# Performance work log

Measured on AMD Instinct MI355X. Metric: run time of the kernel, lower is better.

Reference implementation:

```python
import jax, jax.numpy as jnp
import numpy as np

EPS = 1e-5
EMBED_DIM = 1024
CTX_DIM = 768
NUM_HEADS = 16
DH = EMBED_DIM // NUM_HEADS
# Faithful to torch source: embed_dim // num_heads ** 0.5 parses as embed_dim // (num_heads**0.5)
SCALE = EMBED_DIM // (NUM_HEADS ** 0.5)  # = 256.0


def ws_conv1x1(x, w, b, mask):
    # weight-standardized 1x1 conv1d: w [O, I, 1], x [B, I, T]
    w2 = w[..., 0]
    mu = jnp.mean(w2, axis=1, keepdims=True)
    var = jnp.var(w2, axis=1, keepdims=True)
    wn = (w2 - mu) * jax.lax.rsqrt(var + EPS)
    y = jnp.einsum('oi,bit->bot', wn, x) + b[None, :, None]
    if mask is not None:
        y = jnp.where(mask, y, 0.0)  # mask [B,1,T] bool
    return y


def layernorm(x, g, b):
    # normalize over last axis
    mu = jnp.mean(x, axis=-1, keepdims=True)
    var = jnp.var(x, axis=-1, keepdims=True)
    return (x - mu) * jax.lax.rsqrt(var + EPS) * g + b


def setup_inputs() -> dict:
    key = jax.random.key(0)
    ks = jax.random.split(key, 16)
    B, T, S = 4, 1024, 1024
    inp = {
        'x': jax.random.normal(ks[0], (B, EMBED_DIM, T), dtype=jnp.float32),
        'context': jax.random.normal(ks[1], (B, CTX_DIM, S), dtype=jnp.float32),
        'mask': jax.random.randint(ks[2], (B, 1, T), 0, 2).astype(bool),
        'mask_ctx': jax.random.randint(ks[3], (B, 1, S), 0, 2).astype(bool),
        'qw': jax.random.normal(ks[4], (EMBED_DIM, EMBED_DIM, 1), dtype=jnp.float32) * 0.02,
        'qb': jnp.zeros((EMBED_DIM,), jnp.float32),
        'kw': jax.random.normal(ks[5], (EMBED_DIM, CTX_DIM, 1), dtype=jnp.float32) * 0.02,
        'kb': jnp.zeros((EMBED_DIM,), jnp.float32),
        'vw': jax.random.normal(ks[6], (EMBED_DIM, CTX_DIM, 1), dtype=jnp.float32) * 0.02,
        'vb': jnp.zeros((EMBED_DIM,), jnp.float32),
        'ow': jax.random.normal(ks[7], (EMBED_DIM, EMBED_DIM, 1), dtype=jnp.float32) * 0.02,
        'ob': jnp.zeros((EMBED_DIM,), jnp.float32),
        'gq': jnp.ones((DH,), jnp.float32), 'bq': jnp.zeros((DH,), jnp.float32),
        'gk': jnp.ones((DH,), jnp.float32), 'bk': jnp.zeros((DH,), jnp.float32),
        'gv': jnp.ones((DH,), jnp.float32), 'bv': jnp.zeros((DH,), jnp.float32),
    }
    return inp


def reference(x, context, mask, mask_ctx, qw, qb, kw, kb, vw, vb, ow, ob, gq, bq, gk, bk, gv, bv):
    B, E, T = x.shape
    S = context.shape[-1]
    q = ws_conv1x1(x, qw, qb, mask)            # [B,E,T]
    k = ws_conv1x1(context, kw, kb, mask_ctx)  # [B,E,S]
    v = ws_conv1x1(context, vw, vb, mask_ctx)  # [B,E,S]
    # split heads -> [B,H,dh,L]
    q = q.reshape(B, NUM_HEADS, DH, T)
    k = k.reshape(B, NUM_HEADS, DH, S)
    v = v.reshape(B, NUM_HEADS, DH, S)
    # middle_norm: LayerNorm over dh (applied on transposed layout)
    q = jnp.swapaxes(layernorm(jnp.swapaxes(q, -1, -2), gq, bq), -1, -2)
    k = jnp.swapaxes(layernorm(jnp.swapaxes(k, -1, -2), gk, bk), -1, -2)
    v = jnp.swapaxes(layernorm(jnp.swapaxes(v, -1, -2), gv, bv), -1, -2)
    # scores: k^T @ q -> [B,H,S,T]
    scores = jnp.einsum('bhds,bhdt->bhst', k, q) / SCALE
    scores = jnp.where(mask[:, :, None, :], scores, -1e9)  # mask over query dim T
    scores = jax.nn.softmax(scores, axis=-1)               # softmax over T (as in source)
    scores = jnp.where(mask_ctx[:, :, :, None], scores, 0.0)
    out = jnp.einsum('bhds,bhst->bhdt', v, scores)          # v @ scores -> [B,H,dh,T]
    out = out.reshape(B, E, T)
    out = ws_conv1x1(out, ow, ob, mask) + x
    return out
```

## Files before the change

kernel.cpp:

```cpp
#include <hip/hip_runtime.h>

#define NB 4
#define TT 1024
#define SS 1024
#define EE 1024
#define CCH 768
#define NH 16
#define DHH 64
#define EPSF 1e-5f
#define QSCALE (1.4426950408889634f / 256.0f)

typedef unsigned short u16;
typedef __attribute__((ext_vector_type(8))) short short8;
typedef __attribute__((ext_vector_type(8))) unsigned short u16x8;
typedef __attribute__((ext_vector_type(4))) unsigned short u16x4;
typedef __attribute__((ext_vector_type(4))) float f32x4;

__device__ __forceinline__ u16 f2bu(float f) {
    union { float f; unsigned u; } x; x.f = f;
    unsigned r = x.u + 0x7fffu + ((x.u >> 16) & 1u);
    return (u16)(r >> 16);
}
__device__ __forceinline__ float bu2f(u16 u) {
    union { unsigned u; float f; } x; x.u = ((unsigned)u) << 16; return x.f;
}

#if __has_builtin(__builtin_amdgcn_exp2f)
#define EXP2(x) __builtin_amdgcn_exp2f(x)
#else
#define EXP2(x) exp2f(x)
#endif

#define MFMA16(a, b, c) __builtin_amdgcn_mfma_f32_16x16x32_bf16((a), (b), (c), 0, 0, 0)

__global__ __launch_bounds__(256) void ws_norm4(
    const float* __restrict__ qw, const float* __restrict__ kw,
    const float* __restrict__ vw, const float* __restrict__ ow,
    u16* __restrict__ wqn, u16* __restrict__ wkn,
    u16* __restrict__ wvn, u16* __restrict__ won) {
    int mat = blockIdx.y;
    const float* w = mat == 0 ? qw : (mat == 1 ? kw : (mat == 2 ? vw : ow));
    u16* wn = mat == 0 ? wqn : (mat == 1 ? wkn : (mat == 2 ? wvn : won));
    int I = (mat == 1 || mat == 2) ? CCH : EE;
    int row = blockIdx.x;
    const float* wr = w + (size_t)row * I;
    float s = 0.f, s2 = 0.f;
    for (int i = threadIdx.x; i < I; i += 256) { float v = wr[i]; s += v; s2 += v * v; }
#pragma unroll
    for (int off = 32; off > 0; off >>= 1) { s += __shfl_down(s, off); s2 += __shfl_down(s2, off); }
    __shared__ float sa[4], sb[4], smean, srstd;
    int wid = threadIdx.x >> 6;
    if ((threadIdx.x & 63) == 0) { sa[wid] = s; sb[wid] = s2; }
    __syncthreads();
    if (threadIdx.x == 0) {
        float ts = sa[0] + sa[1] + sa[2] + sa[3];
        float ts2 = sb[0] + sb[1] + sb[2] + sb[3];
        float mean = ts / (float)I;
        float var = ts2 / (float)I - mean * mean;
        smean = mean; srstd = rsqrtf(var + EPSF);
    }
    __syncthreads();
    float mean = smean, r = srstd;
    u16* wo = wn + (size_t)row * I;
    for (int i = threadIdx.x; i < I; i += 256) wo[i] = f2bu((wr[i] - mean) * r);
}

__global__ __launch_bounds__(256) void transpose2_f2b(
    const float* __restrict__ x, const float* __restrict__ ctx,
    u16* __restrict__ xT, u16* __restrict__ cT) {
    __shared__ float tile[64][65];
    int yy = blockIdx.y;
    int mat = yy < 16 ? 0 : 1;
    int r0 = (mat == 0 ? yy : yy - 16) * 64;
    int R = mat == 0 ? EE : CCH;
    const float* in = mat == 0 ? x : ctx;
    u16* out = mat == 0 ? xT : cT;
    int c0 = blockIdx.x * 64, b = blockIdx.z;
    const float* ip = in + (size_t)b * R * 1024;
    u16* op = out + (size_t)b * R * 1024;
    int tid = threadIdx.x;
#pragma unroll
    for (int m = 0; m < 16; m++) {
        int id = tid + 256 * m; int r = id >> 6, c = id & 63;
        tile[r][c] = ip[(size_t)(r0 + r) * 1024 + c0 + c];
    }
    __syncthreads();
#pragma unroll
    for (int m = 0; m < 16; m++) {
        int id = tid + 256 * m; int rr = id >> 6, cc = id & 63;
        op[(size_t)(c0 + rr) * R + r0 + cc] = f2bu(tile[cc][rr]);
    }
}

__device__ __forceinline__ void gemm_core(
    const u16* __restrict__ A, const u16* __restrict__ Bp, int I,
    int o0, int l0, u16 (*at)[72], u16 (*bt)[72], f32x4 (&acc)[4][2]) {
    int tid = threadIdx.x;
    int w = tid >> 6, lane = tid & 63, quad = lane >> 4, l16 = lane & 15;
    int wm = w & 1, wn = w >> 1;
    int rA = tid >> 3, cA = (tid & 7) * 8;
    u16x8 ra[2][4], rb[2][2];
#pragma unroll
    for (int p = 0; p < 2; p++) {
        int kb = p * 64;
#pragma unroll
        for (int m = 0; m < 4; m++)
            ra[p][m] = *(const u16x8*)&A[(size_t)(o0 + rA + 32 * m) * I + kb + cA];
#pragma unroll
        for (int m = 0; m < 2; m++)
            rb[p][m] = *(const u16x8*)&Bp[(size_t)(l0 + rA + 32 * m) * I + kb + cA];
    }
    for (int k0 = 0; k0 < I; k0 += 128) {
#pragma unroll
        for (int half = 0; half < 2; half++) {
            __syncthreads();
#pragma unroll
            for (int m = 0; m < 4; m++) *(u16x8*)&at[rA + 32 * m][cA] = ra[half][m];
#pragma unroll
            for (int m = 0; m < 2; m++) *(u16x8*)&bt[rA + 32 * m][cA] = rb[half][m];
            __syncthreads();
            int kpre = k0 + half * 64 + 128;
            if (kpre < I) {
#pragma unroll
                for (int m = 0; m < 4; m++)
                    ra[half][m] = *(const u16x8*)&A[(size_t)(o0 + rA + 32 * m) * I + kpre + cA];
#pragma unroll
                for (int m = 0; m < 2; m++)
                    rb[half][m] = *(const u16x8*)&Bp[(size_t)(l0 + rA + 32 * m) * I + kpre + cA];
            }
#pragma unroll
            for (int ks = 0; ks < 64; ks += 32) {
                short8 af[4], bf[2];
#pragma unroll
                for (int i = 0; i < 4; i++)
                    af[i] = *(const short8*)&at[wm * 64 + i * 16 + l16][ks + quad * 8];
#pragma unroll
                for (int j = 0; j < 2; j++)
                    bf[j] = *(const short8*)&bt[wn * 32 + j * 16 + l16][ks + quad * 8];
#pragma unroll
                for (int mt = 0; mt < 4; mt++)
#pragma unroll
                    for (int nt = 0; nt < 2; nt++)
                        acc[mt][nt] = MFMA16(af[mt], bf[nt], acc[mt][nt]);
            }
        }
    }
}

__global__ __launch_bounds__(256) void proj_qkv(
    const u16* __restrict__ wq, const u16* __restrict__ wk, const u16* __restrict__ wv,
    const u16* __restrict__ xT, const u16* __restrict__ cT,
    const float* __restrict__ qb, const float* __restrict__ kb, const float* __restrict__ vbi,
    const int* __restrict__ mask_t, const int* __restrict__ mask_c,
    const float* __restrict__ gq, const float* __restrict__ bq,
    const float* __restrict__ gk, const float* __restrict__ bk,
    u16* __restrict__ qT, u16* __restrict__ kT, u16* __restrict__ yv) {
    __shared__ u16 at[128][72];
    __shared__ u16 bt[64][72];
    __shared__ float sg[64], sbe[64], sbias[128];
    int tid = threadIdx.x;
    int w = tid >> 6, lane = tid & 63, quad = lane >> 4, l16 = lane & 15;
    int wm = w & 1, wn = w >> 1;
    int mat = blockIdx.y >> 3;
    int o0 = (blockIdx.y & 7) * 128;
    int l0 = blockIdx.x * 64;
    int b = blockIdx.z;
    const u16* A = mat == 0 ? wq : (mat == 1 ? wk : wv);
    const u16* BT = mat == 0 ? xT : cT;
    const float* bias = mat == 0 ? qb : (mat == 1 ? kb : vbi);
    const int* maskp = mat == 0 ? mask_t : mask_c;
    int I = mat == 0 ? EE : CCH;
    if (mat < 2 && tid < 64) {
        sg[tid] = (mat == 0 ? gq : gk)[tid];
        sbe[tid] = (mat == 0 ? bq : bk)[tid];
    }
    if (tid < 128) sbias[tid] = bias[o0 + tid];

    f32x4 acc[4][2] = {};
    gemm_core(A, BT + (size_t)b * 1024 * I, I, o0, l0, at, bt, acc);

    const int* mrow = maskp + (size_t)b * 1024;
    if (mat < 2) {
        u16* outT = mat == 0 ? qT : kT;
        float scale = mat == 0 ? QSCALE : 1.0f;
        int h = (o0 >> 6) + wm;
        int bh = b * NH + h;
#pragma unroll
        for (int nt = 0; nt < 2; nt++) {
            int l = l0 + wn * 32 + nt * 16 + l16;
            int mval = mrow[l];
            float vbuf[16];
            float s = 0.f;
#pragma unroll
            for (int mt = 0; mt < 4; mt++)
#pragma unroll
                for (int reg = 0; reg < 4; reg++) {
                    float v = mval ? (acc[mt][nt][reg] + sbias[wm * 64 + mt * 16 + quad * 4 + reg]) : 0.f;
                    vbuf[mt * 4 + reg] = v; s += v;
                }
            s += __shfl_xor(s, 16); s += __shfl_xor(s, 32);
            float mean = s * (1.f / 64);
            float s2 = 0.f;
#pragma unroll
            for (int i = 0; i < 16; i++) { float dv = vbuf[i] - mean; s2 += dv * dv; }
            s2 += __shfl_xor(s2, 16); s2 += __shfl_xor(s2, 32);
            float r = rsqrtf(s2 * (1.f / 64) + EPSF);
            u16* op = outT + ((size_t)bh * 1024 + l) * 64;
#pragma unroll
            for (int mt = 0; mt < 4; mt++) {
                u16x4 pk;
#pragma unroll
                for (int reg = 0; reg < 4; reg++) {
                    int d = mt * 16 + quad * 4 + reg;
                    pk[reg] = f2bu(((vbuf[mt * 4 + reg] - mean) * r * sg[d] + sbe[d]) * scale);
                }
                *(u16x4*)&op[mt * 16 + quad * 4] = pk;
            }
        }
    } else {
#pragma unroll
        for (int nt = 0; nt < 2; nt++) {
            int l = l0 + wn * 32 + nt * 16 + l16;
            int mval = mrow[l];
#pragma unroll
            for (int mt = 0; mt < 4; mt++)
#pragma unroll
                for (int reg = 0; reg < 4; reg++) {
                    int o = o0 + wm * 64 + mt * 16 + quad * 4 + reg;
                    float v = mval ? (acc[mt][nt][reg] + sbias[wm * 64 + mt * 16 + quad * 4 + reg]) : 0.f;
                    yv[((size_t)b * EE + o) * 1024 + l] = f2bu(v);
                }
        }
    }
}

__global__ __launch_bounds__(256) void proj_o(
    const u16* __restrict__ won, const u16* __restrict__ aT,
    const float* __restrict__ obi, const int* __restrict__ mask,
    const float* __restrict__ x, float* __restrict__ out) {
    __shared__ u16 at[128][72];
    __shared__ u16 bt[64][72];
    __shared__ float sbias[128];
    int tid = threadIdx.x;
    int w = tid >> 6, lane = tid & 63, quad = lane >> 4, l16 = lane & 15;
    int wm = w & 1, wn = w >> 1;
    int o0 = blockIdx.y * 128, l0 = blockIdx.x * 64, b = blockIdx.z;
    if (tid < 128) sbias[tid] = obi[o0 + tid];
    f32x4 acc[4][2] = {};
    gemm_core(won, aT + (size_t)b * TT * EE, EE, o0, l0, at, bt, acc);
    const int* mrow = mask + (size_t)b * TT;
#pragma unroll
    for (int nt = 0; nt < 2; nt++) {
        int l = l0 + wn * 32 + nt * 16 + l16;
        int mval = mrow[l];
#pragma unroll
        for (int mt = 0; mt < 4; mt++)
#pragma unroll
            for (int reg = 0; reg < 4; reg++) {
                int o = o0 + wm * 64 + mt * 16 + quad * 4 + reg;
                float v = mval ? (acc[mt][nt][reg] + sbias[wm * 64 + mt * 16 + quad * 4 + reg]) : 0.f;
                size_t off = ((size_t)b * EE + o) * TT + l;
                out[off] = v + x[off];
            }
    }
}

__global__ __launch_bounds__(256) void attn_stats_mfma(
    const u16* __restrict__ qT, const u16* __restrict__ kT,
    const int* __restrict__ mask, const int* __restrict__ mask_ctx,
    const float* __restrict__ gv, const float* __restrict__ bv,
    u16* __restrict__ yv) {
    __shared__ u16 kt[64][72];
    __shared__ u16 qt[64][72];
    __shared__ float lp[4][64];
    int tid = threadIdx.x;
    int w = tid >> 6, lane = tid & 63, quad = lane >> 4, l16 = lane & 15;
    int s0 = blockIdx.x * 64, h = blockIdx.y, b = blockIdx.z;
    int head = b * NH + h;
    const u16* kp = kT + (size_t)head * SS * DHH;
    const u16* qp = qT + (size_t)head * TT * DHH;
    const int* mk = mask + (size_t)b * TT;
    int rA = tid >> 3, cA = (tid & 7) * 8;
#pragma unroll
    for (int m = 0; m < 2; m++)
        *(u16x8*)&kt[rA + 32 * m][cA] = *(const u16x8*)&kp[(size_t)(s0 + rA + 32 * m) * DHH + cA];
    u16x8 rq[2][2];
#pragma unroll
    for (int p = 0; p < 2; p++)
#pragma unroll
        for (int m = 0; m < 2; m++)
            rq[p][m] = *(const u16x8*)&qp[(size_t)(p * 64 + rA + 32 * m) * DHH + cA];
    float rl[4][4] = {};
    for (int t0 = 0; t0 < TT; t0 += 128) {
#pragma unroll
        for (int half = 0; half < 2; half++) {
            int tb = t0 + half * 64;
            __syncthreads();
#pragma unroll
            for (int m = 0; m < 2; m++) *(u16x8*)&qt[rA + 32 * m][cA] = rq[half][m];
            __syncthreads();
            int tpre = tb + 128;
            if (tpre < TT) {
#pragma unroll
                for (int m = 0; m < 2; m++)
                    rq[half][m] = *(const u16x8*)&qp[(size_t)(tpre + rA + 32 * m) * DHH + cA];
            }
            int mval = mk[tb + w * 16 + l16];
            f32x4 acc[4] = {};
#pragma unroll
            for (int ks = 0; ks < 64; ks += 32) {
                short8 bf = *(const short8*)&qt[w * 16 + l16][ks + quad * 8];
#pragma unroll
                for (int mt = 0; mt < 4; mt++) {
                    short8 af = *(const short8*)&kt[mt * 16 + l16][ks + quad * 8];
                    acc[mt] = MFMA16(af, bf, acc[mt]);
                }
            }
            if (mval) {
#pragma unroll
                for (int mt = 0; mt < 4; mt++)
#pragma unroll
                    for (int reg = 0; reg < 4; reg++)
                        rl[mt][reg] += EXP2(acc[mt][reg]);
            }
        }
    }
#pragma unroll
    for (int mt = 0; mt < 4; mt++) {
#pragma unroll
        for (int reg = 0; reg < 4; reg++) {
            float v = rl[mt][reg];
            v += __shfl_xor(v, 1); v += __shfl_xor(v, 2);
            v += __shfl_xor(v, 4); v += __shfl_xor(v, 8);
            if (l16 == 0) lp[w][mt * 16 + quad * 4 + reg] = v;
        }
    }
    __syncthreads();
    if (tid < 64) {
        int s = s0 + tid;
        float lv = lp[0][tid] + lp[1][tid] + lp[2][tid] + lp[3][tid];
        int mc = mask_ctx[(size_t)b * SS + s];
        float wsc = (mc != 0 && lv > 0.f) ? (1.f / lv) : 0.f;
        u16* vcol = yv + ((size_t)b * EE + h * 64) * SS + s;
        float sm = 0.f, s2 = 0.f;
#pragma unroll
        for (int d = 0; d < DHH; d++) {
            float v = bu2f(vcol[(size_t)d * SS]);
            sm += v; s2 += v * v;
        }
        float mean = sm * (1.f / DHH);
        float var = s2 * (1.f / DHH) - mean * mean;
        float r = rsqrtf(var + EPSF);
#pragma unroll
        for (int d = 0; d < DHH; d++) {
            float v = bu2f(vcol[(size_t)d * SS]);
            vcol[(size_t)d * SS] = f2bu(((v - mean) * r * gv[d] + bv[d]) * wsc);
        }
    }
}

__global__ __launch_bounds__(256) void attn_pv_mfma(
    const u16* __restrict__ qT, const u16* __restrict__ kT, const u16* __restrict__ vs,
    const int* __restrict__ mask, u16* __restrict__ aT) {
    __shared__ u16 qt[64][72];
    __shared__ u16 kt[64][72];
    __shared__ u16 vt[64][72];
    __shared__ u16 pt[64][72];
    int tid = threadIdx.x;
    int w = tid >> 6, lane = tid & 63, quad = lane >> 4, l16 = lane & 15;
    int t0 = blockIdx.x * 64, h = blockIdx.y, b = blockIdx.z;
    int head = b * NH + h;
    const u16* qp = qT + (size_t)head * TT * DHH;
    const u16* kp = kT + (size_t)head * SS * DHH;
    const u16* vp = vs + ((size_t)head * DHH) * SS;
    int rA = tid >> 3, cA = (tid & 7) * 8;
#pragma unroll
    for (int m = 0; m < 2; m++)
        *(u16x8*)&qt[rA + 32 * m][cA] = *(const u16x8*)&qp[(size_t)(t0 + rA + 32 * m) * DHH + cA];
    u16x8 rk[2][2], rv[2][2];
#pragma unroll
    for (int p = 0; p < 2; p++)
#pragma unroll
        for (int m = 0; m < 2; m++) {
            rk[p][m] = *(const u16x8*)&kp[(size_t)(p * 64 + rA + 32 * m) * DHH + cA];
            rv[p][m] = *(const u16x8*)&vp[(size_t)(rA + 32 * m) * SS + p * 64 + cA];
        }
    int mkv = mask[(size_t)b * TT + t0 + w * 16 + l16];
    int tl = w * 16 + l16;

    f32x4 oacc[4] = {};
    for (int s0 = 0; s0 < SS; s0 += 128) {
#pragma unroll
        for (int half = 0; half < 2; half++) {
            int sb = s0 + half * 64;
            __syncthreads();
#pragma unroll
            for (int m = 0; m < 2; m++) {
                *(u16x8*)&kt[rA + 32 * m][cA] = rk[half][m];
                *(u16x8*)&vt[rA + 32 * m][cA] = rv[half][m];
            }
            __syncthreads();
            int spre = sb + 128;
            if (spre < SS) {
#pragma unroll
                for (int m = 0; m < 2; m++) {
                    rk[half][m] = *(const u16x8*)&kp[(size_t)(spre + rA + 32 * m) * DHH + cA];
                    rv[half][m] = *(const u16x8*)&vp[(size_t)(rA + 32 * m) * SS + spre + cA];
                }
            }
            f32x4 acc[4] = {};
#pragma unroll
            for (int ks = 0; ks < 64; ks += 32) {
                short8 bf = *(const short8*)&qt[tl][ks + quad * 8];
#pragma unroll
                for (int mt = 0; mt < 4; mt++) {
                    short8 af = *(const short8*)&kt[mt * 16 + l16][ks + quad * 8];
                    acc[mt] = MFMA16(af, bf, acc[mt]);
                }
            }
#pragma unroll
            for (int mt = 0; mt < 4; mt++) {
                u16x4 pk;
#pragma unroll
                for (int reg = 0; reg < 4; reg++)
                    pk[reg] = mkv ? f2bu(EXP2(acc[mt][reg])) : (u16)0;
                *(u16x4*)&pt[tl][mt * 16 + quad * 4] = pk;
            }
#pragma unroll
            for (int ks = 0; ks < 64; ks += 32) {
                short8 bf = *(const short8*)&pt[tl][ks + quad * 8];
#pragma unroll
                for (int mt = 0; mt < 4; mt++) {
                    short8 af = *(const short8*)&vt[mt * 16 + l16][ks + quad * 8];
                    oacc[mt] = MFMA16(af, bf, oacc[mt]);
                }
            }
        }
    }
    __syncthreads();
#pragma unroll
    for (int mt = 0; mt < 4; mt++) {
        u16x4 pk;
#pragma unroll
        for (int reg = 0; reg < 4; reg++) pk[reg] = f2bu(oacc[mt][reg]);
        *(u16x4*)&pt[tl][mt * 16 + quad * 4] = pk;
    }
    __syncthreads();
#pragma unroll
    for (int i = 0; i < 2; i++) {
        int id = tid * 2 + i;
        int r = id >> 3, c = (id & 7) * 8;
        *(u16x8*)&aT[((size_t)b * TT + t0 + r) * EE + h * 64 + c] =
            *(const u16x8*)&pt[r][c];
    }
}

extern "C" void kernel_launch(void* const* d_in, const int* in_sizes, int n_in,
                              void* d_out, int out_size, void* d_ws, size_t ws_size,
                              hipStream_t stream) {
    const float* x        = (const float*)d_in[0];
    const float* ctx      = (const float*)d_in[1];
    const int*   mask     = (const int*)d_in[2];
    const int*   mask_ctx = (const int*)d_in[3];
    const float* qw  = (const float*)d_in[4];
    const float* qbi = (const float*)d_in[5];
    const float* kw  = (const float*)d_in[6];
    const float* kbi = (const float*)d_in[7];
    const float* vw  = (const float*)d_in[8];
    const float* vbi = (const float*)d_in[9];
    const float* ow  = (const float*)d_in[10];
    const float* obi = (const float*)d_in[11];
    const float* gq = (const float*)d_in[12];
    const float* bq = (const float*)d_in[13];
    const float* gk = (const float*)d_in[14];
    const float* bk = (const float*)d_in[15];
    const float* gv = (const float*)d_in[16];
    const float* bv = (const float*)d_in[17];

    u16* p = (u16*)d_ws;
    u16* wqn = p; p += (size_t)EE * EE;
    u16* wkn = p; p += (size_t)EE * CCH;
    u16* wvn = p; p += (size_t)EE * CCH;
    u16* won = p; p += (size_t)EE * EE;
    u16* xT  = p; p += (size_t)NB * TT * EE;
    u16* cT  = p; p += (size_t)NB * SS * CCH;
    u16* yv  = p; p += (size_t)NB * EE * SS;
    u16* qT  = p; p += (size_t)NB * NH * TT * DHH;
    u16* kT  = p; p += (size_t)NB * NH * SS * DHH;
    u16* aT  = p; p += (size_t)NB * TT * EE;

    ws_norm4<<<dim3(1024, 4), 256, 0, stream>>>(qw, kw, vw, ow, wqn, wkn, wvn, won);

    transpose2_f2b<<<dim3(16, 28, NB), 256, 0, stream>>>(x, ctx, xT, cT);

    proj_qkv<<<dim3(16, 24, NB), 256, 0, stream>>>(
        wqn, wkn, wvn, xT, cT, qbi, kbi, vbi, mask, mask_ctx,
        gq, bq, gk, bk, qT, kT, yv);

    attn_stats_mfma<<<dim3(SS / 64, NH, NB), 256, 0, stream>>>(
        qT, kT, mask, mask_ctx, gv, bv, yv);

    attn_pv_mfma<<<dim3(TT / 64, NH, NB), 256, 0, stream>>>(qT, kT, yv, mask, aT);

    proj_o<<<dim3(16, 8, NB), 256, 0, stream>>>(won, aT, obi, mask, x, (float*)d_out);
}
```

Measured before the change: 255.1 us.

## Compact masked query/context positions to skip masked attention work

A new prefix-scan kernel turns the query and context masks into compacted position and index arrays plus per-batch counts. The Q/K projections write only unmasked rows, into compacted slots. The stats and PV attention kernels then loop only over the valid counts and exit early for blocks past them, and the output is scattered back to the real query rows. This removes the score, exp and PV computation for masked positions, at the cost of an extra small launch and index indirection. Tail tiles past the counts read unwritten compacted memory, which is zeroed or bounded by count checks.

```diff
diff --git a/kernel.cpp b/kernel.cpp
--- a/kernel.cpp
+++ b/kernel.cpp
@@ -32,6 +32,43 @@
 #endif
 
 #define MFMA16(a, b, c) __builtin_amdgcn_mfma_f32_16x16x32_bf16((a), (b), (c), 0, 0, 0)
+
+__global__ __launch_bounds__(256) void mask_scan(
+    const int* __restrict__ mask, const int* __restrict__ mask_ctx,
+    int* __restrict__ posQ, int* __restrict__ posK,
+    int* __restrict__ tIdx, int* __restrict__ sIdx,
+    int* __restrict__ cntQ, int* __restrict__ cntK) {
+    int which = blockIdx.x & 1, b = blockIdx.x >> 1;
+    const int* m = (which ? mask_ctx : mask) + b * 1024;
+    int* pos = (which ? posK : posQ) + b * 1024;
+    int* idx = (which ? sIdx : tIdx) + b * 1024;
+    int* cnt = (which ? cntK : cntQ) + b;
+    int tid = threadIdx.x;
+    int base = tid * 4;
+    int v[4]; int s = 0;
+#pragma unroll
+    for (int i = 0; i < 4; i++) { v[i] = m[base + i] ? 1 : 0; s += v[i]; }
+    int lane = tid & 63, wid = tid >> 6;
+    int inc = s;
+#pragma unroll
+    for (int off = 1; off < 64; off <<= 1) {
+        int o = __shfl_up(inc, off);
+        if (lane >= off) inc += o;
+    }
+    __shared__ int wtot[4];
+    if (lane == 63) wtot[wid] = inc;
+    __syncthreads();
+    int woff = 0;
+    for (int i = 0; i < wid; i++) woff += wtot[i];
+    int p = woff + inc - s;
+#pragma unroll
+    for (int i = 0; i < 4; i++) {
+        pos[base + i] = p;
+        if (v[i]) idx[p] = base + i;
+        p += v[i];
+    }
+    if (tid == 255) *cnt = p;
+}
 
 __global__ __launch_bounds__(256) void ws_norm4(
     const float* __restrict__ qw, const float* __restrict__ kw,
@@ -152,9 +189,10 @@
     const u16* __restrict__ xT, const u16* __restrict__ cT,
     const float* __restrict__ qb, const float* __restrict__ kb, const float* __restrict__ vbi,
     const int* __restrict__ mask_t, const int* __restrict__ mask_c,
+    const int* __restrict__ posQ, const int* __restrict__ posK,
     const float* __restrict__ gq, const float* __restrict__ bq,
     const float* __restrict__ gk, const float* __restrict__ bk,
-    u16* __restrict__ qT, u16* __restrict__ kT, u16* __restrict__ yv) {
+    u16* __restrict__ qc, u16* __restrict__ kc, u16* __restrict__ yv) {
     __shared__ u16 at[128][72];
     __shared__ u16 bt[64][72];
     __shared__ float sg[64], sbe[64], sbias[128];
@@ -181,7 +219,8 @@
 
     const int* mrow = maskp + (size_t)b * 1024;
     if (mat < 2) {
-        u16* outT = mat == 0 ? qT : kT;
+        u16* outT = mat == 0 ? qc : kc;
+        const int* posArr = (mat == 0 ? posQ : posK) + (size_t)b * 1024;
         float scale = mat == 0 ? QSCALE : 1.0f;
         int h = (o0 >> 6) + wm;
         int bh = b * NH + h;
@@ -205,16 +244,19 @@
             for (int i = 0; i < 16; i++) { float dv = vbuf[i] - mean; s2 += dv * dv; }
             s2 += __shfl_xor(s2, 16); s2 += __shfl_xor(s2, 32);
             float r = rsqrtf(s2 * (1.f / 64) + EPSF);
-            u16* op = outT + ((size_t)bh * 1024 + l) * 64;
-#pragma unroll
-            for (int mt = 0; mt < 4; mt++) {
-                u16x4 pk;
-#pragma unroll
-                for (int reg = 0; reg < 4; reg++) {
-                    int d = mt * 16 + quad * 4 + reg;
-                    pk[reg] = f2bu(((vbuf[mt * 4 + reg] - mean) * r * sg[d] + sbe[d]) * scale);
-                }
-                *(u16x4*)&op[mt * 16 + quad * 4] = pk;
+            if (mval) {
+                int pos = posArr[l];
+                u16* op = outT + ((size_t)bh * 1024 + pos) * 64;
+#pragma unroll
+                for (int mt = 0; mt < 4; mt++) {
+                    u16x4 pk;
+#pragma unroll
+                    for (int reg = 0; reg < 4; reg++) {
+                        int d = mt * 16 + quad * 4 + reg;
+                        pk[reg] = f2bu(((vbuf[mt * 4 + reg] - mean) * r * sg[d] + sbe[d]) * scale);
+                    }
+                    *(u16x4*)&op[mt * 16 + quad * 4] = pk;
+                }
             }
         }
     } else {
@@ -266,20 +308,21 @@
 }
 
 __global__ __launch_bounds__(256) void attn_stats_mfma(
-    const u16* __restrict__ qT, const u16* __restrict__ kT,
-    const int* __restrict__ mask, const int* __restrict__ mask_ctx,
+    const u16* __restrict__ qc, const u16* __restrict__ kc,
+    const int* __restrict__ sIdx, const int* __restrict__ cntQ, const int* __restrict__ cntK,
     const float* __restrict__ gv, const float* __restrict__ bv,
-    u16* __restrict__ yv) {
+    const u16* __restrict__ yv, u16* __restrict__ vc) {
+    int s0 = blockIdx.x * 64, h = blockIdx.y, b = blockIdx.z;
+    int Sc = cntK[b], Tc = cntQ[b];
+    if (s0 >= Sc) return;
     __shared__ u16 kt[64][72];
     __shared__ u16 qt[64][72];
     __shared__ float lp[4][64];
     int tid = threadIdx.x;
     int w = tid >> 6, lane = tid & 63, quad = lane >> 4, l16 = lane & 15;
-    int s0 = blockIdx.x * 64, h = blockIdx.y, b = blockIdx.z;
     int head = b * NH + h;
-    const u16* kp = kT + (size_t)head * SS * DHH;
-    const u16* qp = qT + (size_t)head * TT * DHH;
-    const int* mk = mask + (size_t)b * TT;
+    const u16* kp = kc + (size_t)head * SS * DHH;
+    const u16* qp = qc + (size_t)head * TT * DHH;
     int rA = tid >> 3, cA = (tid & 7) * 8;
 #pragma unroll
     for (int m = 0; m < 2; m++)
@@ -291,7 +334,7 @@
         for (int m = 0; m < 2; m++)
             rq[p][m] = *(const u16x8*)&qp[(size_t)(p * 64 + rA + 32 * m) * DHH + cA];
     float rl[4][4] = {};
-    for (int t0 = 0; t0 < TT; t0 += 128) {
+    for (int t0 = 0; t0 < Tc; t0 += 128) {
 #pragma unroll
         for (int half = 0; half < 2; half++) {
             int tb = t0 + half * 64;
@@ -305,7 +348,7 @@
                 for (int m = 0; m < 2; m++)
                     rq[half][m] = *(const u16x8*)&qp[(size_t)(tpre + rA + 32 * m) * DHH + cA];
             }
-            int mval = mk[tb + w * 16 + l16];
+            int tcol = tb + w * 16 + l16;
             f32x4 acc[4] = {};
 #pragma unroll
             for (int ks = 0; ks < 64; ks += 32) {
@@ -316,7 +359,7 @@
                     acc[mt] = MFMA16(af, bf, acc[mt]);
                 }
             }
-            if (mval) {
+            if (tcol < Tc) {
 #pragma unroll
                 for (int mt = 0; mt < 4; mt++)
 #pragma unroll
@@ -336,43 +379,46 @@
         }
     }
     __syncthreads();
-    if (tid < 64) {
-        int s = s0 + tid;
+    if (tid < 64 && s0 + tid < Sc) {
+        int spos = s0 + tid;
         float lv = lp[0][tid] + lp[1][tid] + lp[2][tid] + lp[3][tid];
-        int mc = mask_ctx[(size_t)b * SS + s];
-        float wsc = (mc != 0 && lv > 0.f) ? (1.f / lv) : 0.f;
-        u16* vcol = yv + ((size_t)b * EE + h * 64) * SS + s;
+        float wsc = lv > 0.f ? (1.f / lv) : 0.f;
+        int sreal = sIdx[(size_t)b * 1024 + spos];
+        const u16* vin = yv + ((size_t)b * EE + h * 64) * SS + sreal;
+        u16* vout = vc + ((size_t)b * EE + h * 64) * SS + spos;
         float sm = 0.f, s2 = 0.f;
+        float vals[DHH];
 #pragma unroll
         for (int d = 0; d < DHH; d++) {
-            float v = bu2f(vcol[(size_t)d * SS]);
-            sm += v; s2 += v * v;
+            float v = bu2f(vin[(size_t)d * SS]);
+            vals[d] = v; sm += v; s2 += v * v;
         }
         float mean = sm * (1.f / DHH);
         float var = s2 * (1.f / DHH) - mean * mean;
         float r = rsqrtf(var + EPSF);
 #pragma unroll
-        for (int d = 0; d < DHH; d++) {
-            float v = bu2f(vcol[(size_t)d * SS]);
-            vcol[(size_t)d * SS] = f2bu(((v - mean) * r * gv[d] + bv[d]) * wsc);
-        }
+        for (int d = 0; d < DHH; d++)
+            vout[(size_t)d * SS] = f2bu(((vals[d] - mean) * r * gv[d] + bv[d]) * wsc);
     }
 }
 
 __global__ __launch_bounds__(256) void attn_pv_mfma(
-    const u16* __restrict__ qT, const u16* __restrict__ kT, const u16* __restrict__ vs,
-    const int* __restrict__ mask, u16* __restrict__ aT) {
+    const u16* __restrict__ qc, const u16* __restrict__ kc, const u16* __restrict__ vc,
+    const int* __restrict__ tIdx, const int* __restrict__ cntQ, const int* __restrict__ cntK,
+    u16* __restrict__ aT) {
+    int t0 = blockIdx.x * 64, h = blockIdx.y, b = blockIdx.z;
+    int Tc = cntQ[b], Sc = cntK[b];
+    if (t0 >= Tc) return;
     __shared__ u16 qt[64][72];
     __shared__ u16 kt[64][72];
     __shared__ u16 vt[64][72];
     __shared__ u16 pt[64][72];
     int tid = threadIdx.x;
     int w = tid >> 6, lane = tid & 63, quad = lane >> 4, l16 = lane & 15;
-    int t0 = blockIdx.x * 64, h = blockIdx.y, b = blockIdx.z;
     int head = b * NH + h;
-    const u16* qp = qT + (size_t)head * TT * DHH;
-    const u16* kp = kT + (size_t)head * SS * DHH;
-    const u16* vp = vs + ((size_t)head * DHH) * SS;
+    const u16* qp = qc + (size_t)head * TT * DHH;
+    const u16* kp = kc + (size_t)head * SS * DHH;
+    const u16* vp = vc + ((size_t)head * DHH) * SS;
     int rA = tid >> 3, cA = (tid & 7) * 8;
 #pragma unroll
     for (int m = 0; m < 2; m++)
@@ -385,14 +431,14 @@
             rk[p][m] = *(const u16x8*)&kp[(size_t)(p * 64 + rA + 32 * m) * DHH + cA];
             rv[p][m] = *(const u16x8*)&vp[(size_t)(rA + 32 * m) * SS + p * 64 + cA];
         }
-    int mkv = mask[(size_t)b * TT + t0 + w * 16 + l16];
     int tl = w * 16 + l16;
 
     f32x4 oacc[4] = {};
-    for (int s0 = 0; s0 < SS; s0 += 128) {
+    for (int s0 = 0; s0 < Sc; s0 += 128) {
 #pragma unroll
         for (int half = 0; half < 2; half++) {
             int sb = s0 + half * 64;
+            if (sb >= Sc) break;
             __syncthreads();
 #pragma unroll
             for (int m = 0; m < 2; m++) {
@@ -422,8 +468,10 @@
             for (int mt = 0; mt < 4; mt++) {
                 u16x4 pk;
 #pragma unroll
-                for (int reg = 0; reg < 4; reg++)
-                    pk[reg] = mkv ? f2bu(EXP2(acc[mt][reg])) : (u16)0;
+                for (int reg = 0; reg < 4; reg++) {
+                    int sl = mt * 16 + quad * 4 + reg;
+                    pk[reg] = (sb + sl < Sc) ? f2bu(EXP2(acc[mt][reg])) : (u16)0;
+                }
                 *(u16x4*)&pt[tl][mt * 16 + quad * 4] = pk;
             }
 #pragma unroll
@@ -446,12 +494,16 @@
         *(u16x4*)&pt[tl][mt * 16 + quad * 4] = pk;
     }
     __syncthreads();
+    const int* ti = tIdx + (size_t)b * 1024;
 #pragma unroll
     for (int i = 0; i < 2; i++) {
         int id = tid * 2 + i;
         int r = id >> 3, c = (id & 7) * 8;
-        *(u16x8*)&aT[((size_t)b * TT + t0 + r) * EE + h * 64 + c] =
-            *(const u16x8*)&pt[r][c];
+        if (t0 + r < Tc) {
+            int treal = ti[t0 + r];
+            *(u16x8*)&aT[((size_t)b * TT + treal) * EE + h * 64 + c] =
+                *(const u16x8*)&pt[r][c];
+        }
     }
 }
 
@@ -485,22 +537,32 @@
     u16* xT  = p; p += (size_t)NB * TT * EE;
     u16* cT  = p; p += (size_t)NB * SS * CCH;
     u16* yv  = p; p += (size_t)NB * EE * SS;
-    u16* qT  = p; p += (size_t)NB * NH * TT * DHH;
-    u16* kT  = p; p += (size_t)NB * NH * SS * DHH;
+    u16* qc  = p; p += (size_t)NB * NH * TT * DHH;
+    u16* kc  = p; p += (size_t)NB * NH * SS * DHH;
+    u16* vc  = p; p += (size_t)NB * EE * SS;
     u16* aT  = p; p += (size_t)NB * TT * EE;
+    int* posQ = (int*)p;
+    int* posK = posQ + NB * 1024;
+    int* tIdx = posK + NB * 1024;
+    int* sIdx = tIdx + NB * 1024;
+    int* cntQ = sIdx + NB * 1024;
+    int* cntK = cntQ + NB;
+
+    mask_scan<<<8, 256, 0, stream>>>(mask, mask_ctx, posQ, posK, tIdx, sIdx, cntQ, cntK);
 
     ws_norm4<<<dim3(1024, 4), 256, 0, stream>>>(qw, kw, vw, ow, wqn, wkn, wvn, won);
 
     transpose2_f2b<<<dim3(16, 28, NB), 256, 0, stream>>>(x, ctx, xT, cT);
 
     proj_qkv<<<dim3(16, 24, NB), 256, 0, stream>>>(
-        wqn, wkn, wvn, xT, cT, qbi, kbi, vbi, mask, mask_ctx,
-        gq, bq, gk, bk, qT, kT, yv);
-
-    attn_stats_mfma<<<dim3(SS / 64, NH, NB), 256, 0, stream>>>(
-        qT, kT, mask, mask_ctx, gv, bv, yv);
-
-    attn_pv_mfma<<<dim3(TT / 64, NH, NB), 256, 0, stream>>>(qT, kT, yv, mask, aT);
+        wqn, wkn, wvn, xT, cT, qbi, kbi, vbi, mask, mask_ctx, posQ, posK,
+        gq, bq, gk, bk, qc, kc, yv);
+
+    attn_stats_mfma<<<dim3(16, NH, NB), 256, 0, stream>>>(
+        qc, kc, sIdx, cntQ, cntK, gv, bv, yv, vc);
+
+    attn_pv_mfma<<<dim3(16, NH, NB), 256, 0, stream>>>(
+        qc, kc, vc, tIdx, cntQ, cntK, aT);
 
     proj_o<<<dim3(16, 8, NB), 256, 0, stream>>>(won, aT, obi, mask, x, (float*)d_out);
 }
```

Result: faster. 236.0 us (-7.5%).
